# Performance work log

Measured on AMD Instinct MI355X. Metric: run time of the kernel, lower is better.

Reference implementation:

```python
import jax, jax.numpy as jnp
import numpy as np

INC, OUTC, NHEADS, KSIZE = 256, 256, 8, 5


def setup_inputs() -> dict:
    key = jax.random.key(0)
    k1, k2 = jax.random.split(key, 2)
    x = jax.random.normal(k1, (4, INC, 64, 64), dtype=jnp.float32)
    w_qkv = jax.random.normal(k2, (3 * OUTC, INC), dtype=jnp.float32) * 0.02
    b_qkv = jnp.zeros((3 * OUTC,), dtype=jnp.float32)
    return {"x": x, "w_qkv": w_qkv, "b_qkv": b_qkv}


def reference(x, w_qkv, b_qkv):
    N, Cin, H, W = x.shape
    hd = OUTC // NHEADS
    ofs = KSIZE // 2
    K2 = KSIZE * KSIZE

    # 1x1 conv == pointwise matmul over channels
    qkv = jnp.einsum('nchw,dc->ndhw', x, w_qkv) + b_qkv[None, :, None, None]
    Q = qkv[:, :OUTC]
    K = qkv[:, OUTC:2 * OUTC]
    V = qkv[:, 2 * OUTC:]

    # Zero-pad K/V; track validity so boundary softmax only spans in-bounds
    # positions (the torch code slices smaller windows at borders -> no pad
    # contribution to softmax).
    Kp = jnp.pad(K, ((0, 0), (0, 0), (ofs, ofs), (ofs, ofs)))
    Vp = jnp.pad(V, ((0, 0), (0, 0), (ofs, ofs), (ofs, ofs)))
    valid = jnp.pad(jnp.ones((H, W), dtype=bool), ((ofs, ofs), (ofs, ofs)))

    # Sliding windows via KSIZE^2 static shifted slices: [N,D,H,W,K2]
    k_win = jnp.stack([Kp[:, :, dy:dy + H, dx:dx + W]
                       for dy in range(KSIZE) for dx in range(KSIZE)], axis=-1)
    v_win = jnp.stack([Vp[:, :, dy:dy + H, dx:dx + W]
                       for dy in range(KSIZE) for dx in range(KSIZE)], axis=-1)
    m_win = jnp.stack([valid[dy:dy + H, dx:dx + W]
                       for dy in range(KSIZE) for dx in range(KSIZE)], axis=-1)  # [H,W,K2]

    qh = Q.reshape(N, NHEADS, hd, H, W)
    kh = k_win.reshape(N, NHEADS, hd, H, W, K2)
    vh = v_win.reshape(N, NHEADS, hd, H, W, K2)

    scores = jnp.einsum('ngdhw,ngdhwk->nghwk', qh, kh)          # [N,G,H,W,K2]
    scores = jnp.where(m_win[None, None], scores, -jnp.inf)
    att = jax.nn.softmax(scores, axis=-1)
    out = jnp.einsum('nghwk,ngdhwk->ngdhw', att, vh)            # [N,G,hd,H,W]
    return out.reshape(N, OUTC, H, W)
```

## Files before the change

### kernel.cpp

```cpp
#include <hip/hip_runtime.h>
#include <hip/hip_bf16.h>
#include <math.h>

#define CIN 256
#define COUT 768
#define OUTC 256
#define HH 64
#define WW 64
#define HW 4096

typedef unsigned int uint32;
typedef unsigned short ushort16;

using short8 = __attribute__((ext_vector_type(8))) short;
using f32x4  = __attribute__((ext_vector_type(4))) float;

__device__ inline uint32 pkbf2(float a, float b) {
    __hip_bfloat162 h = __float22bfloat162_rn(make_float2(a, b));
    union { __hip_bfloat162 h2; uint32 u; } cv; cv.h2 = h;
    return cv.u;
}

__device__ inline uint32 pkhf2(float a, float b) {
    union { _Float16 h[2]; uint32 u; } cv;
    cv.h[0] = (_Float16)a; cv.h[1] = (_Float16)b;
    return cv.u;
}

__device__ inline float f16lo(uint32 u) {
    union { uint32 u; _Float16 h[2]; } c; c.u = u; return (float)c.h[0];
}
__device__ inline float f16hi(uint32 u) {
    union { uint32 u; _Float16 h[2]; } c; c.u = u; return (float)c.h[1];
}

__device__ inline float dpp_xor1(float x) {
#if __has_builtin(__builtin_amdgcn_update_dpp)
    int i = __builtin_amdgcn_update_dpp(0, __float_as_int(x),
                                        0xB1, 0xF, 0xF, true);
    return __int_as_float(i);
#else
    return __shfl_xor(x, 1, 64);
#endif
}

__device__ inline void gld16(const void* g, void* l) {
    __builtin_amdgcn_global_load_lds(
        (const __attribute__((address_space(1))) unsigned int*)g,
        (__attribute__((address_space(3))) unsigned int*)l, 16, 0, 0);
}

__global__ __launch_bounds__(256) void cvt_x_kernel(
    const float* __restrict__ x, ushort16* __restrict__ xT)
{
    __shared__ float T[64][65];
    const int n  = blockIdx.z;
    const int c0 = blockIdx.y * 64;
    const int p0 = blockIdx.x * 64;
    const int tid = threadIdx.x;
    const int ty = tid >> 4, tx = tid & 15;

    #pragma unroll
    for (int i = 0; i < 4; ++i) {
        float4 v = *(const float4*)&x[((size_t)(n * CIN + c0 + i * 16 + ty)) * HW + p0 + tx * 4];
        T[i * 16 + ty][tx * 4 + 0] = v.x;
        T[i * 16 + ty][tx * 4 + 1] = v.y;
        T[i * 16 + ty][tx * 4 + 2] = v.z;
        T[i * 16 + ty][tx * 4 + 3] = v.w;
    }
    __syncthreads();

    #pragma unroll
    for (int it = 0; it < 2; ++it) {
        const int t  = it * 256 + tid;
        const int pl = t >> 3, oc = t & 7;
        uint32 u0 = pkbf2(T[oc * 8 + 0][pl], T[oc * 8 + 1][pl]);
        uint32 u1 = pkbf2(T[oc * 8 + 2][pl], T[oc * 8 + 3][pl]);
        uint32 u2 = pkbf2(T[oc * 8 + 4][pl], T[oc * 8 + 5][pl]);
        uint32 u3 = pkbf2(T[oc * 8 + 6][pl], T[oc * 8 + 7][pl]);
        *(uint4*)&xT[((size_t)n * HW + p0 + pl) * CIN + c0 + oc * 8] =
            make_uint4(u0, u1, u2, u3);
    }
}

__global__ __launch_bounds__(256) void cvt_w_kernel(
    const float* __restrict__ wq, ushort16* __restrict__ wb)
{
    const int i = (blockIdx.x * 256 + threadIdx.x) * 8;
    float4 a = *(const float4*)&wq[i];
    float4 b = *(const float4*)&wq[i + 4];
    *(uint4*)&wb[i] = make_uint4(pkbf2(a.x, a.y), pkbf2(a.z, a.w),
                                 pkbf2(b.x, b.y), pkbf2(b.z, b.w));
}

__global__ __launch_bounds__(256) void qkv_gemm2(
    const ushort16* __restrict__ wb, const ushort16* __restrict__ xT,
    const float* __restrict__ bq, ushort16* __restrict__ qkv)
{
    __shared__ ushort16 As[2][128 * 32];
    __shared__ ushort16 Bs[2][128 * 32];

    const int n   = blockIdx.z;
    const int d0  = blockIdx.y * 128;
    const int p0  = blockIdx.x * 128;
    const int tid = threadIdx.x;
    const int lane = tid & 63;
    const int wid  = tid >> 6;
    const int wm = wid >> 1, wn = wid & 1;

    const int srow = lane >> 2;
    const int skk  = (lane & 3) * 8;
    const ushort16* ag = wb + (size_t)(d0 + wid * 32 + srow) * CIN + skk;
    const ushort16* bg = xT + ((size_t)n * HW + p0 + wid * 32 + srow) * CIN + skk;

    const int lrow = lane & 15;
    const int lk   = (lane >> 4) * 8;

    f32x4 acc[4][4];
    #pragma unroll
    for (int i = 0; i < 4; ++i)
        #pragma unroll
        for (int j = 0; j < 4; ++j) acc[i][j] = (f32x4){0.f, 0.f, 0.f, 0.f};

#define STAGE(buf, ko) do {                                              \
        gld16(ag + (ko),            &As[buf][(wid * 32)      * 32]);     \
        gld16(ag + (ko) + 16 * CIN, &As[buf][(wid * 32 + 16) * 32]);     \
        gld16(bg + (ko),            &Bs[buf][(wid * 32)      * 32]);     \
        gld16(bg + (ko) + 16 * CIN, &Bs[buf][(wid * 32 + 16) * 32]);     \
    } while (0)

    STAGE(0, 0);
    __syncthreads();

    int cur = 0;
    #pragma unroll 1
    for (int kt = 0; kt < 8; ++kt) {
        if (kt < 7) STAGE(cur ^ 1, (kt + 1) * 32);

        short8 af[4], bf[4];
        #pragma unroll
        for (int fm = 0; fm < 4; ++fm)
            af[fm] = *(const short8*)&As[cur][(wm * 64 + fm * 16 + lrow) * 32 + lk];
        #pragma unroll
        for (int fn = 0; fn < 4; ++fn)
            bf[fn] = *(const short8*)&Bs[cur][(wn * 64 + fn * 16 + lrow) * 32 + lk];
        #pragma unroll
        for (int fm = 0; fm < 4; ++fm)
            #pragma unroll
            for (int fn = 0; fn < 4; ++fn)
                acc[fm][fn] = __builtin_amdgcn_mfma_f32_16x16x32_bf16(
                    af[fm], bf[fn], acc[fm][fn], 0, 0, 0);

        __syncthreads();
        cur ^= 1;
    }
#undef STAGE

    const int hi4 = lane >> 4;
    ushort16* qn = qkv + (size_t)n * COUT * HW;
    #pragma unroll
    for (int fm = 0; fm < 4; ++fm) {
        const int D = d0 + wm * 64 + fm * 16 + hi4 * 4;
        const float4 bias = *(const float4*)(&bq[D]);
        const int slot = D >> 5, dlow = D & 31;
        ushort16* qs = qn + (size_t)slot * (HW * 32) + dlow;
        #pragma unroll
        for (int fn = 0; fn < 4; ++fn) {
            const int p = p0 + wn * 64 + fn * 16 + lrow;
            f32x4 v = acc[fm][fn];
            uint32 u0 = pkhf2(v[0] + bias.x, v[1] + bias.y);
            uint32 u1 = pkhf2(v[2] + bias.z, v[3] + bias.w);
            *(uint2*)(qs + (size_t)p * 32) = make_uint2(u0, u1);
        }
    }
}

#define TR 4
#define TC 32
#define HR 8
#define HC 36
#define NPIX (HR*HC)

__global__ __launch_bounds__(256) void attn_kernel(
    const ushort16* __restrict__ qkv, float* __restrict__ out)
{
    __shared__ uint4 Ks[NPIX * 4];
    __shared__ uint4 Vs[NPIX * 4];

    const int n    = blockIdx.z;
    const int head = blockIdx.y;
    const int ht = blockIdx.x >> 1;
    const int wt = blockIdx.x & 1;
    const int h0 = ht * TR;
    const int w0 = wt * TC;

    const int tid  = threadIdx.x;
    const int half = tid & 1;
    const int wc   = (tid >> 1) & 31;
    const int tr   = tid >> 6;

    const int h = h0 + tr, w = w0 + wc;
    const int p = h * WW + w;

    const uint4* Kb = (const uint4*)(qkv + ((size_t)(n * 24 + 8 + head)) * HW * 32);
    const uint4* Vb = (const uint4*)(qkv + ((size_t)(n * 24 + 16 + head)) * HW * 32);

    for (int c = tid; c < 2 * NPIX * 4; c += 256) {
        const int b  = (c >= NPIX * 4);
        const int cc = c - b * NPIX * 4;
        const int pix = cc >> 2, i = cc & 3;
        const int hr = pix / HC, cw = pix - hr * HC;
        const int hh = h0 + hr - 2, ww = w0 + cw - 2;
        if (hh >= 0 && hh < HH && ww >= 0 && ww < WW) {
            const int pp = hh * WW + ww;
            const uint4 v = (b ? Vb : Kb)[(size_t)pp * 4 + i];
            const int unit = (pix * 4 + i) ^ (pix & 7);
            (b ? Vs : Ks)[unit] = v;
        }
    }

    float qf[16];
    {
        const uint4* Qp = (const uint4*)(qkv + (((size_t)(n * 24 + head)) * HW + p) * 32);
        #pragma unroll
        for (int i = 0; i < 2; ++i) {
            uint4 u = Qp[half * 2 + i];
            qf[8*i+0] = f16lo(u.x); qf[8*i+1] = f16hi(u.x);
            qf[8*i+2] = f16lo(u.y); qf[8*i+3] = f16hi(u.y);
            qf[8*i+4] = f16lo(u.z); qf[8*i+5] = f16hi(u.z);
            qf[8*i+6] = f16lo(u.w); qf[8*i+7] = f16hi(u.w);
        }
    }

    __syncthreads();

    float sc[25];
    #pragma unroll
    for (int ky = 0; ky < 5; ++ky) {
        const int hh = h + ky - 2;
        const int hr = tr + ky;
        #pragma unroll
        for (int kx = 0; kx < 5; ++kx) {
            const int ww = w + kx - 2;
            float s;
            if (hh >= 0 && hh < HH && ww >= 0 && ww < WW) {
                const int pix = hr * HC + (wc + kx);
                const int u0 = (pix * 4 + half * 2)     ^ (pix & 7);
                const int u1 = (pix * 4 + half * 2 + 1) ^ (pix & 7);
                uint4 a = Ks[u0], b = Ks[u1];
                float t = 0.f;
                t = fmaf(qf[0],  f16lo(a.x), t); t = fmaf(qf[1],  f16hi(a.x), t);
                t = fmaf(qf[2],  f16lo(a.y), t); t = fmaf(qf[3],  f16hi(a.y), t);
                t = fmaf(qf[4],  f16lo(a.z), t); t = fmaf(qf[5],  f16hi(a.z), t);
                t = fmaf(qf[6],  f16lo(a.w), t); t = fmaf(qf[7],  f16hi(a.w), t);
                t = fmaf(qf[8],  f16lo(b.x), t); t = fmaf(qf[9],  f16hi(b.x), t);
                t = fmaf(qf[10], f16lo(b.y), t); t = fmaf(qf[11], f16hi(b.y), t);
                t = fmaf(qf[12], f16lo(b.z), t); t = fmaf(qf[13], f16hi(b.z), t);
                t = fmaf(qf[14], f16lo(b.w), t); t = fmaf(qf[15], f16hi(b.w), t);
                s = t;
            } else {
                s = -1e30f;
            }
            sc[ky * 5 + kx] = s;
        }
    }
    #pragma unroll
    for (int k = 0; k < 25; ++k) {
        float o = dpp_xor1(sc[k]);
        sc[k] = (sc[k] <= -1e29f) ? sc[k] : sc[k] + o;
    }

    float m = sc[0];
    #pragma unroll
    for (int k = 1; k < 25; ++k) m = fmaxf(m, sc[k]);
    float sum = 0.f;
    #pragma unroll
    for (int k = 0; k < 25; ++k) {
        float e = __expf(sc[k] - m);
        sc[k] = e;
        sum += e;
    }
    const float inv = 1.f / sum;

    float al[8], ah[8];
    #pragma unroll
    for (int i = 0; i < 8; ++i) { al[i] = 0.f; ah[i] = 0.f; }
    #pragma unroll
    for (int ky = 0; ky < 5; ++ky) {
        const int hh = h + ky - 2;
        if (hh < 0 || hh >= HH) continue;
        const int hr = tr + ky;
        #pragma unroll
        for (int kx = 0; kx < 5; ++kx) {
            const int ww = w + kx - 2;
            if (ww < 0 || ww >= WW) continue;
            const float a = sc[ky * 5 + kx];
            const int pix = hr * HC + (wc + kx);
            const int u0 = (pix * 4 + half * 2)     ^ (pix & 7);
            const int u1 = (pix * 4 + half * 2 + 1) ^ (pix & 7);
            uint4 x = Vs[u0], y = Vs[u1];
            al[0] = fmaf(a, f16lo(x.x), al[0]); ah[0] = fmaf(a, f16hi(x.x), ah[0]);
            al[1] = fmaf(a, f16lo(x.y), al[1]); ah[1] = fmaf(a, f16hi(x.y), ah[1]);
            al[2] = fmaf(a, f16lo(x.z), al[2]); ah[2] = fmaf(a, f16hi(x.z), ah[2]);
            al[3] = fmaf(a, f16lo(x.w), al[3]); ah[3] = fmaf(a, f16hi(x.w), ah[3]);
            al[4] = fmaf(a, f16lo(y.x), al[4]); ah[4] = fmaf(a, f16hi(y.x), ah[4]);
            al[5] = fmaf(a, f16lo(y.y), al[5]); ah[5] = fmaf(a, f16hi(y.y), ah[5]);
            al[6] = fmaf(a, f16lo(y.z), al[6]); ah[6] = fmaf(a, f16hi(y.z), ah[6]);
            al[7] = fmaf(a, f16lo(y.w), al[7]); ah[7] = fmaf(a, f16hi(y.w), ah[7]);
        }
    }

    float* Ob = out + ((size_t)(n * 8 + head) * 32 + half * 16) * HW + p;
    #pragma unroll
    for (int i = 0; i < 8; ++i) {
        Ob[(size_t)(2*i)   * HW] = al[i] * inv;
        Ob[(size_t)(2*i+1) * HW] = ah[i] * inv;
    }
}

extern "C" void kernel_launch(void* const* d_in, const int* in_sizes, int n_in,
                              void* d_out, int out_size, void* d_ws, size_t ws_size,
                              hipStream_t stream) {
    const float* x  = (const float*)d_in[0];
    const float* wq = (const float*)d_in[1];
    const float* bq = (const float*)d_in[2];
    float* out = (float*)d_out;

    ushort16* qkv = (ushort16*)d_ws;
    ushort16* xT  = (ushort16*)((char*)d_ws + (32u << 20));
    ushort16* wbf = (ushort16*)((char*)d_ws + (44u << 20));

    dim3 g0(HW / 64, CIN / 64, 4);
    cvt_x_kernel<<<g0, 256, 0, stream>>>(x, xT);
    cvt_w_kernel<<<96, 256, 0, stream>>>(wq, wbf);

    dim3 g1(HW / 128, COUT / 128, 4);
    qkv_gemm2<<<g1, 256, 0, stream>>>(wbf, xT, bq, qkv);

    dim3 g2(32, 8, 4);
    attn_kernel<<<g2, 256, 0, stream>>>(qkv, out);
}
```

Before: 49.54 us.

## Fuse conversion, QKV GEMM and attention into one cooperative persistent kernel

Replaces four kernel launches with a single cooperative kernel of 512 persistent blocks that use grid-wide syncs between the conversion, GEMM and attention phases. It reuses one shared memory buffer across phases. The GEMM tile is shrunk to 128x64 so that 1536 tiles spread over the 512 blocks. This removes launch overhead and inter-kernel gaps, but adds grid-sync cost and smaller GEMM tiles with less operand reuse.

```diff
diff --git a/kernel.cpp b/kernel.cpp
--- a/kernel.cpp
+++ b/kernel.cpp
@@ -1,6 +1,9 @@
 #include <hip/hip_runtime.h>
 #include <hip/hip_bf16.h>
+#include <hip/hip_cooperative_groups.h>
 #include <math.h>
+
+namespace cg = cooperative_groups;
 
 #define CIN 256
 #define COUT 768
@@ -20,20 +23,17 @@
     union { __hip_bfloat162 h2; uint32 u; } cv; cv.h2 = h;
     return cv.u;
 }
-
 __device__ inline uint32 pkhf2(float a, float b) {
     union { _Float16 h[2]; uint32 u; } cv;
     cv.h[0] = (_Float16)a; cv.h[1] = (_Float16)b;
     return cv.u;
 }
-
 __device__ inline float f16lo(uint32 u) {
     union { uint32 u; _Float16 h[2]; } c; c.u = u; return (float)c.h[0];
 }
 __device__ inline float f16hi(uint32 u) {
     union { uint32 u; _Float16 h[2]; } c; c.u = u; return (float)c.h[1];
 }
-
 __device__ inline float dpp_xor1(float x) {
 #if __has_builtin(__builtin_amdgcn_update_dpp)
     int i = __builtin_amdgcn_update_dpp(0, __float_as_int(x),
@@ -43,136 +43,10 @@
     return __shfl_xor(x, 1, 64);
 #endif
 }
-
 __device__ inline void gld16(const void* g, void* l) {
     __builtin_amdgcn_global_load_lds(
         (const __attribute__((address_space(1))) unsigned int*)g,
         (__attribute__((address_space(3))) unsigned int*)l, 16, 0, 0);
-}
-
-__global__ __launch_bounds__(256) void cvt_x_kernel(
-    const float* __restrict__ x, ushort16* __restrict__ xT)
-{
-    __shared__ float T[64][65];
-    const int n  = blockIdx.z;
-    const int c0 = blockIdx.y * 64;
-    const int p0 = blockIdx.x * 64;
-    const int tid = threadIdx.x;
-    const int ty = tid >> 4, tx = tid & 15;
-
-    #pragma unroll
-    for (int i = 0; i < 4; ++i) {
-        float4 v = *(const float4*)&x[((size_t)(n * CIN + c0 + i * 16 + ty)) * HW + p0 + tx * 4];
-        T[i * 16 + ty][tx * 4 + 0] = v.x;
-        T[i * 16 + ty][tx * 4 + 1] = v.y;
-        T[i * 16 + ty][tx * 4 + 2] = v.z;
-        T[i * 16 + ty][tx * 4 + 3] = v.w;
-    }
-    __syncthreads();
-
-    #pragma unroll
-    for (int it = 0; it < 2; ++it) {
-        const int t  = it * 256 + tid;
-        const int pl = t >> 3, oc = t & 7;
-        uint32 u0 = pkbf2(T[oc * 8 + 0][pl], T[oc * 8 + 1][pl]);
-        uint32 u1 = pkbf2(T[oc * 8 + 2][pl], T[oc * 8 + 3][pl]);
-        uint32 u2 = pkbf2(T[oc * 8 + 4][pl], T[oc * 8 + 5][pl]);
-        uint32 u3 = pkbf2(T[oc * 8 + 6][pl], T[oc * 8 + 7][pl]);
-        *(uint4*)&xT[((size_t)n * HW + p0 + pl) * CIN + c0 + oc * 8] =
-            make_uint4(u0, u1, u2, u3);
-    }
-}
-
-__global__ __launch_bounds__(256) void cvt_w_kernel(
-    const float* __restrict__ wq, ushort16* __restrict__ wb)
-{
-    const int i = (blockIdx.x * 256 + threadIdx.x) * 8;
-    float4 a = *(const float4*)&wq[i];
-    float4 b = *(const float4*)&wq[i + 4];
-    *(uint4*)&wb[i] = make_uint4(pkbf2(a.x, a.y), pkbf2(a.z, a.w),
-                                 pkbf2(b.x, b.y), pkbf2(b.z, b.w));
-}
-
-__global__ __launch_bounds__(256) void qkv_gemm2(
-    const ushort16* __restrict__ wb, const ushort16* __restrict__ xT,
-    const float* __restrict__ bq, ushort16* __restrict__ qkv)
-{
-    __shared__ ushort16 As[2][128 * 32];
-    __shared__ ushort16 Bs[2][128 * 32];
-
-    const int n   = blockIdx.z;
-    const int d0  = blockIdx.y * 128;
-    const int p0  = blockIdx.x * 128;
-    const int tid = threadIdx.x;
-    const int lane = tid & 63;
-    const int wid  = tid >> 6;
-    const int wm = wid >> 1, wn = wid & 1;
-
-    const int srow = lane >> 2;
-    const int skk  = (lane & 3) * 8;
-    const ushort16* ag = wb + (size_t)(d0 + wid * 32 + srow) * CIN + skk;
-    const ushort16* bg = xT + ((size_t)n * HW + p0 + wid * 32 + srow) * CIN + skk;
-
-    const int lrow = lane & 15;
-    const int lk   = (lane >> 4) * 8;
-
-    f32x4 acc[4][4];
-    #pragma unroll
-    for (int i = 0; i < 4; ++i)
-        #pragma unroll
-        for (int j = 0; j < 4; ++j) acc[i][j] = (f32x4){0.f, 0.f, 0.f, 0.f};
-
-#define STAGE(buf, ko) do {                                              \
-        gld16(ag + (ko),            &As[buf][(wid * 32)      * 32]);     \
-        gld16(ag + (ko) + 16 * CIN, &As[buf][(wid * 32 + 16) * 32]);     \
-        gld16(bg + (ko),            &Bs[buf][(wid * 32)      * 32]);     \
-        gld16(bg + (ko) + 16 * CIN, &Bs[buf][(wid * 32 + 16) * 32]);     \
-    } while (0)
-
-    STAGE(0, 0);
-    __syncthreads();
-
-    int cur = 0;
-    #pragma unroll 1
-    for (int kt = 0; kt < 8; ++kt) {
-        if (kt < 7) STAGE(cur ^ 1, (kt + 1) * 32);
-
-        short8 af[4], bf[4];
-        #pragma unroll
-        for (int fm = 0; fm < 4; ++fm)
-            af[fm] = *(const short8*)&As[cur][(wm * 64 + fm * 16 + lrow) * 32 + lk];
-        #pragma unroll
-        for (int fn = 0; fn < 4; ++fn)
-            bf[fn] = *(const short8*)&Bs[cur][(wn * 64 + fn * 16 + lrow) * 32 + lk];
-        #pragma unroll
-        for (int fm = 0; fm < 4; ++fm)
-            #pragma unroll
-            for (int fn = 0; fn < 4; ++fn)
-                acc[fm][fn] = __builtin_amdgcn_mfma_f32_16x16x32_bf16(
-                    af[fm], bf[fn], acc[fm][fn], 0, 0, 0);
-
-        __syncthreads();
-        cur ^= 1;
-    }
-#undef STAGE
-
-    const int hi4 = lane >> 4;
-    ushort16* qn = qkv + (size_t)n * COUT * HW;
-    #pragma unroll
-    for (int fm = 0; fm < 4; ++fm) {
-        const int D = d0 + wm * 64 + fm * 16 + hi4 * 4;
-        const float4 bias = *(const float4*)(&bq[D]);
-        const int slot = D >> 5, dlow = D & 31;
-        ushort16* qs = qn + (size_t)slot * (HW * 32) + dlow;
-        #pragma unroll
-        for (int fn = 0; fn < 4; ++fn) {
-            const int p = p0 + wn * 64 + fn * 16 + lrow;
-            f32x4 v = acc[fm][fn];
-            uint32 u0 = pkhf2(v[0] + bias.x, v[1] + bias.y);
-            uint32 u1 = pkhf2(v[2] + bias.z, v[3] + bias.w);
-            *(uint2*)(qs + (size_t)p * 32) = make_uint2(u0, u1);
-        }
-    }
 }
 
 #define TR 4
@@ -181,140 +55,287 @@
 #define HC 36
 #define NPIX (HR*HC)
 
-__global__ __launch_bounds__(256) void attn_kernel(
-    const ushort16* __restrict__ qkv, float* __restrict__ out)
+__global__ __launch_bounds__(256, 2) void fused_kernel(
+    const float* __restrict__ x, const float* __restrict__ wq,
+    const float* __restrict__ bq, ushort16* __restrict__ xT,
+    ushort16* __restrict__ wbf, ushort16* __restrict__ qkv,
+    float* __restrict__ out)
 {
-    __shared__ uint4 Ks[NPIX * 4];
-    __shared__ uint4 Vs[NPIX * 4];
-
-    const int n    = blockIdx.z;
-    const int head = blockIdx.y;
-    const int ht = blockIdx.x >> 1;
-    const int wt = blockIdx.x & 1;
-    const int h0 = ht * TR;
-    const int w0 = wt * TC;
-
-    const int tid  = threadIdx.x;
-    const int half = tid & 1;
-    const int wc   = (tid >> 1) & 31;
-    const int tr   = tid >> 6;
-
-    const int h = h0 + tr, w = w0 + wc;
-    const int p = h * WW + w;
-
-    const uint4* Kb = (const uint4*)(qkv + ((size_t)(n * 24 + 8 + head)) * HW * 32);
-    const uint4* Vb = (const uint4*)(qkv + ((size_t)(n * 24 + 16 + head)) * HW * 32);
-
-    for (int c = tid; c < 2 * NPIX * 4; c += 256) {
-        const int b  = (c >= NPIX * 4);
-        const int cc = c - b * NPIX * 4;
-        const int pix = cc >> 2, i = cc & 3;
-        const int hr = pix / HC, cw = pix - hr * HC;
-        const int hh = h0 + hr - 2, ww = w0 + cw - 2;
-        if (hh >= 0 && hh < HH && ww >= 0 && ww < WW) {
-            const int pp = hh * WW + ww;
-            const uint4 v = (b ? Vb : Kb)[(size_t)pp * 4 + i];
-            const int unit = (pix * 4 + i) ^ (pix & 7);
-            (b ? Vs : Ks)[unit] = v;
+    __shared__ __align__(16) char smem[36928];
+
+    const int bid = blockIdx.x;
+    const int tid = threadIdx.x;
+
+    {
+        const int gid = bid * 256 + tid;
+        if (gid < (COUT * CIN / 8)) {
+            const float* s = wq + (size_t)gid * 8;
+            float4 a = *(const float4*)s;
+            float4 b = *(const float4*)(s + 4);
+            *(uint4*)&wbf[(size_t)gid * 8] =
+                make_uint4(pkbf2(a.x, a.y), pkbf2(a.z, a.w),
+                           pkbf2(b.x, b.y), pkbf2(b.z, b.w));
         }
     }
 
-    float qf[16];
     {
-        const uint4* Qp = (const uint4*)(qkv + (((size_t)(n * 24 + head)) * HW + p) * 32);
-        #pragma unroll
-        for (int i = 0; i < 2; ++i) {
-            uint4 u = Qp[half * 2 + i];
-            qf[8*i+0] = f16lo(u.x); qf[8*i+1] = f16hi(u.x);
-            qf[8*i+2] = f16lo(u.y); qf[8*i+3] = f16hi(u.y);
-            qf[8*i+4] = f16lo(u.z); qf[8*i+5] = f16hi(u.z);
-            qf[8*i+6] = f16lo(u.w); qf[8*i+7] = f16hi(u.w);
+        float (*T)[65] = (float(*)[65])smem;
+        const int ty = tid >> 4, tx = tid & 15;
+        #pragma unroll 1
+        for (int it = 0; it < 2; ++it) {
+            const int t  = bid + it * 512;
+            const int n  = t >> 8;
+            const int c0 = ((t >> 6) & 3) * 64;
+            const int p0 = (t & 63) * 64;
+            __syncthreads();
+            #pragma unroll
+            for (int i = 0; i < 4; ++i) {
+                float4 v = *(const float4*)&x[((size_t)(n * CIN + c0 + i * 16 + ty)) * HW + p0 + tx * 4];
+                T[i * 16 + ty][tx * 4 + 0] = v.x;
+                T[i * 16 + ty][tx * 4 + 1] = v.y;
+                T[i * 16 + ty][tx * 4 + 2] = v.z;
+                T[i * 16 + ty][tx * 4 + 3] = v.w;
+            }
+            __syncthreads();
+            #pragma unroll
+            for (int j = 0; j < 2; ++j) {
+                const int tt = j * 256 + tid;
+                const int pl = tt >> 3, oc = tt & 7;
+                uint32 u0 = pkbf2(T[oc * 8 + 0][pl], T[oc * 8 + 1][pl]);
+                uint32 u1 = pkbf2(T[oc * 8 + 2][pl], T[oc * 8 + 3][pl]);
+                uint32 u2 = pkbf2(T[oc * 8 + 4][pl], T[oc * 8 + 5][pl]);
+                uint32 u3 = pkbf2(T[oc * 8 + 6][pl], T[oc * 8 + 7][pl]);
+                *(uint4*)&xT[((size_t)n * HW + p0 + pl) * CIN + c0 + oc * 8] =
+                    make_uint4(u0, u1, u2, u3);
+            }
         }
     }
 
-    __syncthreads();
-
-    float sc[25];
-    #pragma unroll
-    for (int ky = 0; ky < 5; ++ky) {
-        const int hh = h + ky - 2;
-        const int hr = tr + ky;
-        #pragma unroll
-        for (int kx = 0; kx < 5; ++kx) {
-            const int ww = w + kx - 2;
-            float s;
-            if (hh >= 0 && hh < HH && ww >= 0 && ww < WW) {
-                const int pix = hr * HC + (wc + kx);
-                const int u0 = (pix * 4 + half * 2)     ^ (pix & 7);
-                const int u1 = (pix * 4 + half * 2 + 1) ^ (pix & 7);
-                uint4 a = Ks[u0], b = Ks[u1];
-                float t = 0.f;
-                t = fmaf(qf[0],  f16lo(a.x), t); t = fmaf(qf[1],  f16hi(a.x), t);
-                t = fmaf(qf[2],  f16lo(a.y), t); t = fmaf(qf[3],  f16hi(a.y), t);
-                t = fmaf(qf[4],  f16lo(a.z), t); t = fmaf(qf[5],  f16hi(a.z), t);
-                t = fmaf(qf[6],  f16lo(a.w), t); t = fmaf(qf[7],  f16hi(a.w), t);
-                t = fmaf(qf[8],  f16lo(b.x), t); t = fmaf(qf[9],  f16hi(b.x), t);
-                t = fmaf(qf[10], f16lo(b.y), t); t = fmaf(qf[11], f16hi(b.y), t);
-                t = fmaf(qf[12], f16lo(b.z), t); t = fmaf(qf[13], f16hi(b.z), t);
-                t = fmaf(qf[14], f16lo(b.w), t); t = fmaf(qf[15], f16hi(b.w), t);
-                s = t;
-            } else {
-                s = -1e30f;
-            }
-            sc[ky * 5 + kx] = s;
+    cg::this_grid().sync();
+
+    {
+        ushort16* As = (ushort16*)smem;
+        ushort16* Bs = (ushort16*)smem + 8192;
+        const int lane = tid & 63;
+        const int wid  = tid >> 6;
+        const int wm = wid >> 1, wn = wid & 1;
+        const int lrow = lane & 15;
+        const int lk   = (lane >> 4) * 8;
+        const int srow = lane >> 2;
+        const int skk  = (lane & 3) * 8;
+
+        #pragma unroll 1
+        for (int it = 0; it < 3; ++it) {
+            const int t   = bid + it * 512;
+            const int dt  = t >> 8;
+            const int rem = t & 255;
+            const int n   = rem >> 6;
+            const int pt  = rem & 63;
+            const int d0  = dt * 128;
+            const int p0  = pt * 64;
+
+            const ushort16* ag = wbf + (size_t)(d0 + wid * 32 + srow) * CIN + skk;
+            const ushort16* bg = xT + ((size_t)n * HW + p0 + wid * 16 + srow) * CIN + skk;
+
+            f32x4 acc[4][2];
+            #pragma unroll
+            for (int i = 0; i < 4; ++i)
+                #pragma unroll
+                for (int j = 0; j < 2; ++j) acc[i][j] = (f32x4){0.f, 0.f, 0.f, 0.f};
+
+#define STG(buf, ko) do {                                                     \
+            gld16(ag + (ko),            As + (buf) * 4096 + (wid * 32) * 32); \
+            gld16(ag + (ko) + 16 * CIN, As + (buf) * 4096 + (wid * 32 + 16) * 32); \
+            gld16(bg + (ko),            Bs + (buf) * 2048 + (wid * 16) * 32); \
+        } while (0)
+
+            __syncthreads();
+            STG(0, 0);
+            __syncthreads();
+
+            int cur = 0;
+            #pragma unroll 1
+            for (int kt = 0; kt < 8; ++kt) {
+                if (kt < 7) STG(cur ^ 1, (kt + 1) * 32);
+
+                short8 af[4], bf[2];
+                #pragma unroll
+                for (int fm = 0; fm < 4; ++fm)
+                    af[fm] = *(const short8*)(As + cur * 4096 + (wm * 64 + fm * 16 + lrow) * 32 + lk);
+                #pragma unroll
+                for (int fn = 0; fn < 2; ++fn)
+                    bf[fn] = *(const short8*)(Bs + cur * 2048 + (wn * 32 + fn * 16 + lrow) * 32 + lk);
+                #pragma unroll
+                for (int fm = 0; fm < 4; ++fm)
+                    #pragma unroll
+                    for (int fn = 0; fn < 2; ++fn)
+                        acc[fm][fn] = __builtin_amdgcn_mfma_f32_16x16x32_bf16(
+                            af[fm], bf[fn], acc[fm][fn], 0, 0, 0);
+
+                __syncthreads();
+                cur ^= 1;
+            }
+#undef STG
+
+            const int hi4 = lane >> 4;
+            ushort16* qn = qkv + (size_t)n * COUT * HW;
+            #pragma unroll
+            for (int fm = 0; fm < 4; ++fm) {
+                const int D = d0 + wm * 64 + fm * 16 + hi4 * 4;
+                const float4 bias = *(const float4*)(&bq[D]);
+                const int slot = D >> 5, dlow = D & 31;
+                ushort16* qs = qn + (size_t)slot * (HW * 32) + dlow;
+                #pragma unroll
+                for (int fn = 0; fn < 2; ++fn) {
+                    const int p = p0 + wn * 32 + fn * 16 + lrow;
+                    f32x4 v = acc[fm][fn];
+                    uint32 u0 = pkhf2(v[0] + bias.x, v[1] + bias.y);
+                    uint32 u1 = pkhf2(v[2] + bias.z, v[3] + bias.w);
+                    *(uint2*)(qs + (size_t)p * 32) = make_uint2(u0, u1);
+                }
+            }
         }
     }
-    #pragma unroll
-    for (int k = 0; k < 25; ++k) {
-        float o = dpp_xor1(sc[k]);
-        sc[k] = (sc[k] <= -1e29f) ? sc[k] : sc[k] + o;
-    }
-
-    float m = sc[0];
-    #pragma unroll
-    for (int k = 1; k < 25; ++k) m = fmaxf(m, sc[k]);
-    float sum = 0.f;
-    #pragma unroll
-    for (int k = 0; k < 25; ++k) {
-        float e = __expf(sc[k] - m);
-        sc[k] = e;
-        sum += e;
-    }
-    const float inv = 1.f / sum;
-
-    float al[8], ah[8];
-    #pragma unroll
-    for (int i = 0; i < 8; ++i) { al[i] = 0.f; ah[i] = 0.f; }
-    #pragma unroll
-    for (int ky = 0; ky < 5; ++ky) {
-        const int hh = h + ky - 2;
-        if (hh < 0 || hh >= HH) continue;
-        const int hr = tr + ky;
-        #pragma unroll
-        for (int kx = 0; kx < 5; ++kx) {
-            const int ww = w + kx - 2;
-            if (ww < 0 || ww >= WW) continue;
-            const float a = sc[ky * 5 + kx];
-            const int pix = hr * HC + (wc + kx);
-            const int u0 = (pix * 4 + half * 2)     ^ (pix & 7);
-            const int u1 = (pix * 4 + half * 2 + 1) ^ (pix & 7);
-            uint4 x = Vs[u0], y = Vs[u1];
-            al[0] = fmaf(a, f16lo(x.x), al[0]); ah[0] = fmaf(a, f16hi(x.x), ah[0]);
-            al[1] = fmaf(a, f16lo(x.y), al[1]); ah[1] = fmaf(a, f16hi(x.y), ah[1]);
-            al[2] = fmaf(a, f16lo(x.z), al[2]); ah[2] = fmaf(a, f16hi(x.z), ah[2]);
-            al[3] = fmaf(a, f16lo(x.w), al[3]); ah[3] = fmaf(a, f16hi(x.w), ah[3]);
-            al[4] = fmaf(a, f16lo(y.x), al[4]); ah[4] = fmaf(a, f16hi(y.x), ah[4]);
-            al[5] = fmaf(a, f16lo(y.y), al[5]); ah[5] = fmaf(a, f16hi(y.y), ah[5]);
-            al[6] = fmaf(a, f16lo(y.z), al[6]); ah[6] = fmaf(a, f16hi(y.z), ah[6]);
-            al[7] = fmaf(a, f16lo(y.w), al[7]); ah[7] = fmaf(a, f16hi(y.w), ah[7]);
+
+    cg::this_grid().sync();
+
+    {
+        uint4* Ks = (uint4*)smem;
+        uint4* Vs = Ks + NPIX * 4;
+
+        const int half = tid & 1;
+        const int wc   = (tid >> 1) & 31;
+        const int tr   = tid >> 6;
+
+        #pragma unroll 1
+        for (int it = 0; it < 2; ++it) {
+            const int t    = bid + it * 512;
+            const int n    = t >> 8;
+            const int head = (t >> 5) & 7;
+            const int tl   = t & 31;
+            const int h0   = (tl >> 1) * TR;
+            const int w0   = (tl & 1) * TC;
+
+            const int h = h0 + tr, w = w0 + wc;
+            const int p = h * WW + w;
+
+            const uint4* Kb = (const uint4*)(qkv + ((size_t)(n * 24 + 8 + head)) * HW * 32);
+            const uint4* Vb = (const uint4*)(qkv + ((size_t)(n * 24 + 16 + head)) * HW * 32);
+
+            __syncthreads();
+
+            for (int c = tid; c < 2 * NPIX * 4; c += 256) {
+                const int b  = (c >= NPIX * 4);
+                const int cc = c - b * NPIX * 4;
+                const int pix = cc >> 2, i = cc & 3;
+                const int hr = pix / HC, cw = pix - hr * HC;
+                const int hh = h0 + hr - 2, ww = w0 + cw - 2;
+                if (hh >= 0 && hh < HH && ww >= 0 && ww < WW) {
+                    const int pp = hh * WW + ww;
+                    const uint4 v = (b ? Vb : Kb)[(size_t)pp * 4 + i];
+                    const int unit = (pix * 4 + i) ^ (pix & 7);
+                    (b ? Vs : Ks)[unit] = v;
+                }
+            }
+
+            float qf[16];
+            {
+                const uint4* Qp = (const uint4*)(qkv + (((size_t)(n * 24 + head)) * HW + p) * 32);
+                #pragma unroll
+                for (int i = 0; i < 2; ++i) {
+                    uint4 u = Qp[half * 2 + i];
+                    qf[8*i+0] = f16lo(u.x); qf[8*i+1] = f16hi(u.x);
+                    qf[8*i+2] = f16lo(u.y); qf[8*i+3] = f16hi(u.y);
+                    qf[8*i+4] = f16lo(u.z); qf[8*i+5] = f16hi(u.z);
+                    qf[8*i+6] = f16lo(u.w); qf[8*i+7] = f16hi(u.w);
+                }
+            }
+
+            __syncthreads();
+
+            float sc[25];
+            #pragma unroll
+            for (int ky = 0; ky < 5; ++ky) {
+                const int hh = h + ky - 2;
+                const int hr = tr + ky;
+                #pragma unroll
+                for (int kx = 0; kx < 5; ++kx) {
+                    const int ww = w + kx - 2;
+                    float s;
+                    if (hh >= 0 && hh < HH && ww >= 0 && ww < WW) {
+                        const int pix = hr * HC + (wc + kx);
+                        const int u0 = (pix * 4 + half * 2)     ^ (pix & 7);
+                        const int u1 = (pix * 4 + half * 2 + 1) ^ (pix & 7);
+                        uint4 a = Ks[u0], b = Ks[u1];
+                        float tt = 0.f;
+                        tt = fmaf(qf[0],  f16lo(a.x), tt); tt = fmaf(qf[1],  f16hi(a.x), tt);
+                        tt = fmaf(qf[2],  f16lo(a.y), tt); tt = fmaf(qf[3],  f16hi(a.y), tt);
+                        tt = fmaf(qf[4],  f16lo(a.z), tt); tt = fmaf(qf[5],  f16hi(a.z), tt);
+                        tt = fmaf(qf[6],  f16lo(a.w), tt); tt = fmaf(qf[7],  f16hi(a.w), tt);
+                        tt = fmaf(qf[8],  f16lo(b.x), tt); tt = fmaf(qf[9],  f16hi(b.x), tt);
+                        tt = fmaf(qf[10], f16lo(b.y), tt); tt = fmaf(qf[11], f16hi(b.y), tt);
+                        tt = fmaf(qf[12], f16lo(b.z), tt); tt = fmaf(qf[13], f16hi(b.z), tt);
+                        tt = fmaf(qf[14], f16lo(b.w), tt); tt = fmaf(qf[15], f16hi(b.w), tt);
+                        s = tt;
+                    } else {
+                        s = -1e30f;
+                    }
+                    sc[ky * 5 + kx] = s;
+                }
+            }
+            #pragma unroll
+            for (int k = 0; k < 25; ++k) {
+                float o = dpp_xor1(sc[k]);
+                sc[k] = (sc[k] <= -1e29f) ? sc[k] : sc[k] + o;
+            }
+
+            float m = sc[0];
+            #pragma unroll
+            for (int k = 1; k < 25; ++k) m = fmaxf(m, sc[k]);
+            float sum = 0.f;
+            #pragma unroll
+            for (int k = 0; k < 25; ++k) {
+                float e = __expf(sc[k] - m);
+                sc[k] = e;
+                sum += e;
+            }
+            const float inv = 1.f / sum;
+
+            float al[8], ah[8];
+            #pragma unroll
+            for (int i = 0; i < 8; ++i) { al[i] = 0.f; ah[i] = 0.f; }
+            #pragma unroll
+            for (int ky = 0; ky < 5; ++ky) {
+                const int hh = h + ky - 2;
+                if (hh < 0 || hh >= HH) continue;
+                const int hr = tr + ky;
+                #pragma unroll
+                for (int kx = 0; kx < 5; ++kx) {
+                    const int ww = w + kx - 2;
+                    if (ww < 0 || ww >= WW) continue;
+                    const float a = sc[ky * 5 + kx];
+                    const int pix = hr * HC + (wc + kx);
+                    const int u0 = (pix * 4 + half * 2)     ^ (pix & 7);
+                    const int u1 = (pix * 4 + half * 2 + 1) ^ (pix & 7);
+                    uint4 xv = Vs[u0], yv = Vs[u1];
+                    al[0] = fmaf(a, f16lo(xv.x), al[0]); ah[0] = fmaf(a, f16hi(xv.x), ah[0]);
+                    al[1] = fmaf(a, f16lo(xv.y), al[1]); ah[1] = fmaf(a, f16hi(xv.y), ah[1]);
+                    al[2] = fmaf(a, f16lo(xv.z), al[2]); ah[2] = fmaf(a, f16hi(xv.z), ah[2]);
+                    al[3] = fmaf(a, f16lo(xv.w), al[3]); ah[3] = fmaf(a, f16hi(xv.w), ah[3]);
+                    al[4] = fmaf(a, f16lo(yv.x), al[4]); ah[4] = fmaf(a, f16hi(yv.x), ah[4]);
+                    al[5] = fmaf(a, f16lo(yv.y), al[5]); ah[5] = fmaf(a, f16hi(yv.y), ah[5]);
+                    al[6] = fmaf(a, f16lo(yv.z), al[6]); ah[6] = fmaf(a, f16hi(yv.z), ah[6]);
+                    al[7] = fmaf(a, f16lo(yv.w), al[7]); ah[7] = fmaf(a, f16hi(yv.w), ah[7]);
+                }
+            }
+
+            float* Ob = out + ((size_t)(n * 8 + head) * 32 + half * 16) * HW + p;
+            #pragma unroll
+            for (int i = 0; i < 8; ++i) {
+                Ob[(size_t)(2*i)   * HW] = al[i] * inv;
+                Ob[(size_t)(2*i+1) * HW] = ah[i] * inv;
+            }
         }
-    }
-
-    float* Ob = out + ((size_t)(n * 8 + head) * 32 + half * 16) * HW + p;
-    #pragma unroll
-    for (int i = 0; i < 8; ++i) {
-        Ob[(size_t)(2*i)   * HW] = al[i] * inv;
-        Ob[(size_t)(2*i+1) * HW] = ah[i] * inv;
     }
 }
 
@@ -324,19 +345,14 @@
     const float* x  = (const float*)d_in[0];
     const float* wq = (const float*)d_in[1];
     const float* bq = (const float*)d_in[2];
-    float* out = (float*)d_out;
+    float* outp = (float*)d_out;
 
     ushort16* qkv = (ushort16*)d_ws;
     ushort16* xT  = (ushort16*)((char*)d_ws + (32u << 20));
     ushort16* wbf = (ushort16*)((char*)d_ws + (44u << 20));
 
-    dim3 g0(HW / 64, CIN / 64, 4);
-    cvt_x_kernel<<<g0, 256, 0, stream>>>(x, xT);
-    cvt_w_kernel<<<96, 256, 0, stream>>>(wq, wbf);
-
-    dim3 g1(HW / 128, COUT / 128, 4);
-    qkv_gemm2<<<g1, 256, 0, stream>>>(wbf, xT, bq, qkv);
-
-    dim3 g2(32, 8, 4);
-    attn_kernel<<<g2, 256, 0, stream>>>(qkv, out);
-}
+    void* args[] = { (void*)&x, (void*)&wq, (void*)&bq, (void*)&xT,
+                     (void*)&wbf, (void*)&qkv, (void*)&outp };
+    hipLaunchCooperativeKernel((void*)fused_kernel, dim3(512), dim3(256),
+                               args, 0, stream);
+}
```

New measurement: 191.8 us. +287.1%, slower.
